# Optimization experiments

Hardware: AMD Instinct MI355X
Metric: run time of the kernel (lower is better)

Reference implementation:

```python
import jax, jax.numpy as jnp
import numpy as np
from jax import lax

N, C_IN, L = 32, 8, 4096
C_LAT, K_EMB, E_DIM = 64, 512, 64
KSZ, STRIDE, PAD = 4, 2, 2


def setup_inputs() -> dict:
    key = jax.random.key(0)
    ks = jax.random.split(key, 6)
    s_conv = 1.0 / np.sqrt(C_IN * KSZ)
    s_tconv = 1.0 / np.sqrt(C_LAT * KSZ)
    return {
        "x": jax.random.normal(ks[0], (N, C_IN, L), jnp.float32),
        "conv_w": jax.random.normal(ks[1], (C_LAT, C_IN, KSZ), jnp.float32) * s_conv,
        "conv_b": jax.random.normal(ks[2], (C_LAT,), jnp.float32) * s_conv,
        "codebook": jax.random.normal(ks[3], (K_EMB, E_DIM), jnp.float32),
        "tconv_w": jax.random.normal(ks[4], (C_LAT, C_IN, KSZ), jnp.float32) * s_tconv,
        "tconv_b": jax.random.normal(ks[5], (C_IN,), jnp.float32) * s_tconv,
    }


def _encode(x, conv_w, conv_b):
    z = lax.conv_general_dilated(
        x, conv_w, window_strides=(STRIDE,), padding=[(PAD, PAD)],
        dimension_numbers=("NCH", "OIH", "NCH"))
    return z + conv_b[None, :, None]


def _quantize(z_e, codebook):
    n, c, l = z_e.shape
    z_flat = z_e.transpose(0, 2, 1).reshape(-1, c)          # (n*l, c)
    z_sq = jnp.sum(z_flat * z_flat, axis=1, keepdims=True)  # (n*l, 1)
    cb_sq = jnp.sum(codebook * codebook, axis=1)            # (k,)
    dist = z_sq + cb_sq[None, :] - 2.0 * (z_flat @ codebook.T)
    indices = jnp.argmin(dist, axis=-1)                     # (n*l,)
    z_q = codebook[indices].reshape(n, l, c).transpose(0, 2, 1)
    return z_q, indices.reshape(n, l)


def _decode(z_q, tconv_w, tconv_b):
    # torch ConvTranspose1d == conv with lhs-dilated input, flipped/transposed kernel
    w_t = jnp.flip(tconv_w, -1).transpose(1, 0, 2)          # (out, in, k)
    x_rec = lax.conv_general_dilated(
        z_q, w_t, window_strides=(1,),
        padding=[(KSZ - 1 - PAD, KSZ - 1 - PAD)],
        lhs_dilation=(STRIDE,),
        dimension_numbers=("NCH", "OIH", "NCH"))
    return x_rec + tconv_b[None, :, None]


def reference(x, conv_w, conv_b, codebook, tconv_w, tconv_b):
    z_e = _encode(x, conv_w, conv_b)            # (N, C_LAT, L/2+1)
    z_q, indices = _quantize(z_e, codebook)
    x_recon = _decode(z_q, tconv_w, tconv_b)    # (N, C_IN, L)
    return x_recon, z_e, z_q, indices
```

## Files before the change

### kernel.cpp

```cpp
#include <hip/hip_runtime.h>
#include <stdint.h>

#define N_B   32
#define C_INN 8
#define L_IN  4096
#define C_LAT 64
#define K_EMB 512
#define E_DIM 64
#define L_OUT 2049
#define M_ROWS (N_B * L_OUT)

#define SZ_XREC (N_B * C_INN * L_IN)
#define SZ_ZE   (N_B * C_LAT * L_OUT)
#define OFF_XREC 0
#define OFF_ZE   (SZ_XREC)
#define OFF_ZQ   (OFF_ZE + SZ_ZE)
#define OFF_IDX  (OFF_ZQ + SZ_ZE)

typedef short short8 __attribute__((ext_vector_type(8)));
typedef float f32x4  __attribute__((ext_vector_type(4)));

__device__ __forceinline__ unsigned short rne16(float f) {
    unsigned u = __float_as_uint(f);
    return (unsigned short)((u + 0x7FFFu + ((u >> 16) & 1u)) >> 16);
}
__device__ __forceinline__ float frombits16(unsigned short h) {
    return __uint_as_float(((unsigned)h) << 16);
}
__device__ __forceinline__ unsigned orderbits(float f) {
    unsigned u = __float_as_uint(f);
    return u ^ ((unsigned)((int)u >> 31) | 0x80000000u);
}

__global__ __launch_bounds__(256) void prep_kernel(
    const float* __restrict__ cb, unsigned short* __restrict__ frag,
    float* __restrict__ cbh)
{
    const int ntile = blockIdx.x;
    const int t     = threadIdx.x;
    const int lane  = t & 63;
    const int ks    = (t >> 6) & 1;
    const int h     = t >> 7;
    const int code  = ntile * 16 + (lane & 15);
    const int k0    = ks * 32 + (lane >> 4) * 8;

    const float* src = cb + (size_t)code * E_DIM + k0;
    unsigned short out[8];
#pragma unroll
    for (int j = 0; j < 8; ++j) {
        const float v = src[j];
        const unsigned short hb = rne16(v);
        out[j] = h ? rne16(v - frombits16(hb)) : hb;
    }
    short8 v8;
#pragma unroll
    for (int j = 0; j < 8; ++j) v8[j] = (short)out[j];
    short8* dst = (short8*)(frag + (((size_t)(ntile * 2 + ks) * 2 + h) * 512 + lane * 8));
    *dst = v8;

    if (t < 16) {
        const int c2 = ntile * 16 + t;
        const float4* cp = (const float4*)(cb + (size_t)c2 * E_DIM);
        float s = 0.0f;
#pragma unroll
        for (int d = 0; d < E_DIM / 4; ++d) {
            float4 v = cp[d];
            s += v.x * v.x + v.y * v.y + v.z * v.z + v.w * v.w;
        }
        cbh[c2] = 0.5f * s;
    }
}

__global__ __launch_bounds__(256, 3) void quantize_kernel(
    const float* __restrict__ x, const float* __restrict__ conv_w,
    const float* __restrict__ conv_b, const float* __restrict__ cb,
    const unsigned short* __restrict__ frag, const float* __restrict__ cbh_ws,
    float* __restrict__ z_e, float* __restrict__ z_q,
    float* __restrict__ idx_out)
{
    __shared__ float s_z[E_DIM][66];
    __shared__ float s_cbh[K_EMB];
    __shared__ unsigned s_cand[64][68];
    __shared__ float s_znorm[64];
    __shared__ unsigned s_mstar[64];
    __shared__ unsigned long long s_final[64];
    __shared__ unsigned s_list[256];
    __shared__ int s_cnt;

    const int tid  = threadIdx.x;
    const int wave = tid >> 6;
    const int lane = tid & 63;
    const int p    = wave >> 1;
    const int h    = wave & 1;

    s_cbh[tid]       = cbh_ws[tid];
    s_cbh[tid + 256] = cbh_ws[tid + 256];
    if (tid < 64) s_final[tid] = ~0ULL;
    if (tid == 0) s_cnt = 0;

    const int  row    = lane;
    const int  r      = blockIdx.x * 64 + row;
    const bool active = (r < M_ROWS);
    const unsigned rr = active ? (unsigned)r : 0u;
    const unsigned n  = rr / 2049u;
    const unsigned tt = rr - n * 2049u;

    {
        const float* xrow = x + (size_t)n * (C_INN * L_IN);
        float xv[C_INN][4];
        const bool fast = (tt >= 1 && tt <= 2047);
        if (fast) {
#pragma unroll
            for (int ci = 0; ci < C_INN; ++ci) {
                float4 v = *(const float4*)(xrow + ci * L_IN + (2 * (int)tt - 2));
                xv[ci][0] = v.x; xv[ci][1] = v.y; xv[ci][2] = v.z; xv[ci][3] = v.w;
            }
        } else {
#pragma unroll
            for (int ci = 0; ci < C_INN; ++ci) {
#pragma unroll
                for (int k = 0; k < 4; ++k) {
                    int xi = 2 * (int)tt - 2 + k;
                    int xc = min(max(xi, 0), L_IN - 1);
                    float v = xrow[ci * L_IN + xc];
                    xv[ci][k] = (xi >= 0 && xi < L_IN) ? v : 0.0f;
                }
            }
        }
        float* zcol = z_e + (size_t)n * (C_LAT * L_OUT) + tt;
#pragma unroll
        for (int j = 0; j < 16; ++j) {
            const int c = wave * 16 + j;
            float a = conv_b[c];
#pragma unroll
            for (int ci = 0; ci < C_INN; ++ci) {
                const float* wp = conv_w + (c * C_INN + ci) * 4;
#pragma unroll
                for (int k = 0; k < 4; ++k) a += xv[ci][k] * wp[k];
            }
            s_z[c][row] = a;
            if (active) zcol[(size_t)c * L_OUT] = a;
        }
    }
    __syncthreads();

    if (tid < 64) {
        float s = 0.0f;
#pragma unroll 8
        for (int c = 0; c < E_DIM; ++c) {
            const float v = s_z[c][tid];
            s += v * v;
        }
        s_znorm[tid] = 0.5f * s + 1.0f;
    }

    const int m = lane & 15, q = lane >> 4;
    short8 Ah[2][2], Al[2][2];
#pragma unroll
    for (int st = 0; st < 2; ++st) {
        const int arow = p * 32 + st * 16 + m;
#pragma unroll
        for (int ks = 0; ks < 2; ++ks) {
#pragma unroll
            for (int j = 0; j < 8; ++j) {
                const float v = -s_z[ks * 32 + q * 8 + j][arow];
                const unsigned short hb = rne16(v);
                Ah[st][ks][j] = (short)hb;
                Al[st][ks][j] = (short)rne16(v - frombits16(hb));
            }
        }
    }
    __syncthreads();

    float Kn[2][4];
#pragma unroll
    for (int st = 0; st < 2; ++st)
#pragma unroll
        for (int r4 = 0; r4 < 4; ++r4)
            Kn[st][r4] = s_znorm[p * 32 + st * 16 + q * 4 + r4];

    unsigned ca[2][4], cb2[2][4];
#pragma unroll
    for (int st = 0; st < 2; ++st)
#pragma unroll
        for (int r4 = 0; r4 < 4; ++r4) { ca[st][r4] = 0xFFFFFFFFu; cb2[st][r4] = 0xFFFFFFFFu; }

    const short8* B8 = (const short8*)frag;
    short8 Bc[4], Bn[4];
    {
        const int base = (h * 16) * 256 + lane;
#pragma unroll
        for (int v = 0; v < 4; ++v) Bc[v] = B8[base + v * 64];
    }

    for (int t = 0; t < 16; ++t) {
        if (t < 15) {
            const int base = (h * 16 + t + 1) * 256 + lane;
#pragma unroll
            for (int v = 0; v < 4; ++v) Bn[v] = B8[base + v * 64];
        }
        const int code = (h * 16 + t) * 16 + m;
        const float chv = s_cbh[code];

        f32x4 accA = {chv + Kn[0][0], chv + Kn[0][1], chv + Kn[0][2], chv + Kn[0][3]};
        f32x4 accB = {chv + Kn[1][0], chv + Kn[1][1], chv + Kn[1][2], chv + Kn[1][3]};
        accA = __builtin_amdgcn_mfma_f32_16x16x32_bf16(Ah[0][0], Bc[0], accA, 0, 0, 0);
        accB = __builtin_amdgcn_mfma_f32_16x16x32_bf16(Ah[1][0], Bc[0], accB, 0, 0, 0);
        accA = __builtin_amdgcn_mfma_f32_16x16x32_bf16(Ah[0][0], Bc[1], accA, 0, 0, 0);
        accB = __builtin_amdgcn_mfma_f32_16x16x32_bf16(Ah[1][0], Bc[1], accB, 0, 0, 0);
        accA = __builtin_amdgcn_mfma_f32_16x16x32_bf16(Al[0][0], Bc[0], accA, 0, 0, 0);
        accB = __builtin_amdgcn_mfma_f32_16x16x32_bf16(Al[1][0], Bc[0], accB, 0, 0, 0);
        accA = __builtin_amdgcn_mfma_f32_16x16x32_bf16(Ah[0][1], Bc[2], accA, 0, 0, 0);
        accB = __builtin_amdgcn_mfma_f32_16x16x32_bf16(Ah[1][1], Bc[2], accB, 0, 0, 0);
        accA = __builtin_amdgcn_mfma_f32_16x16x32_bf16(Ah[0][1], Bc[3], accA, 0, 0, 0);
        accB = __builtin_amdgcn_mfma_f32_16x16x32_bf16(Ah[1][1], Bc[3], accB, 0, 0, 0);
        accA = __builtin_amdgcn_mfma_f32_16x16x32_bf16(Al[0][1], Bc[2], accA, 0, 0, 0);
        accB = __builtin_amdgcn_mfma_f32_16x16x32_bf16(Al[1][1], Bc[2], accB, 0, 0, 0);

#pragma unroll
        for (int st = 0; st < 2; ++st) {
            const f32x4 acc = st ? accB : accA;
#pragma unroll
            for (int r4 = 0; r4 < 4; ++r4) {
                const unsigned xx = (__float_as_uint(acc[r4]) & 0xFFFFFFF0u) | (unsigned)t;
                const unsigned mx = max(ca[st][r4], xx);
                ca[st][r4]  = min(ca[st][r4], xx);
                cb2[st][r4] = min(cb2[st][r4], mx);
            }
        }
#pragma unroll
        for (int v = 0; v < 4; ++v) Bc[v] = Bn[v];
    }

#pragma unroll
    for (int st = 0; st < 2; ++st)
#pragma unroll
        for (int r4 = 0; r4 < 4; ++r4) {
            const int rw = p * 32 + st * 16 + q * 4 + r4;
            s_cand[rw][h * 32 + 2 * m + 0] = ca[st][r4];
            s_cand[rw][h * 32 + 2 * m + 1] = cb2[st][r4];
        }
    __syncthreads();

    if (tid < 64) {
        unsigned mn = 0xFFFFFFFFu;
#pragma unroll 8
        for (int i = 0; i < 64; ++i) mn = min(mn, s_cand[tid][i]);
        s_mstar[tid] = mn & 0xFFFFFFF0u;
    }
    __syncthreads();

    {
        const int rw  = tid >> 2;
        const float thr = __uint_as_float(s_mstar[rw]) + 0.02f;
#pragma unroll
        for (int j = 0; j < 16; ++j) {
            const int sl = (tid & 3) * 16 + j;
            const unsigned cand = s_cand[rw][sl];
            const float fd = __uint_as_float(cand & 0xFFFFFFF0u);
            if (fd <= thr) {
                const unsigned code =
                    (((unsigned)(sl >> 5) * 16u + (cand & 15u)) * 16u) +
                    (unsigned)((sl >> 1) & 15);
                const int pos = atomicAdd(&s_cnt, 1);
                if (pos < 256) {
                    s_list[pos] = ((unsigned)rw << 9) | code;
                } else {
                    const float4* c4 = (const float4*)(cb + (size_t)code * E_DIM);
                    float dot = 0.0f;
#pragma unroll
                    for (int d4 = 0; d4 < 16; ++d4) {
                        const float4 cv = c4[d4];
                        dot += s_z[d4 * 4 + 0][rw] * cv.x +
                               s_z[d4 * 4 + 1][rw] * cv.y +
                               s_z[d4 * 4 + 2][rw] * cv.z +
                               s_z[d4 * 4 + 3][rw] * cv.w;
                    }
                    const float mex = s_cbh[code] - dot;
                    const unsigned long long px =
                        ((unsigned long long)orderbits(mex) << 32) | code;
                    atomicMin(&s_final[rw], px);
                }
            }
        }
    }
    __syncthreads();

    {
        const int nk = min(s_cnt, 256);
        for (int e = tid; e < nk; e += 256) {
            const unsigned ent = s_list[e];
            const int rw = (int)(ent >> 9);
            const unsigned code = ent & 511u;
            const float4* c4 = (const float4*)(cb + (size_t)code * E_DIM);
            float dot = 0.0f;
#pragma unroll
            for (int d4 = 0; d4 < 16; ++d4) {
                const float4 cv = c4[d4];
                dot += s_z[d4 * 4 + 0][rw] * cv.x +
                       s_z[d4 * 4 + 1][rw] * cv.y +
                       s_z[d4 * 4 + 2][rw] * cv.z +
                       s_z[d4 * 4 + 3][rw] * cv.w;
            }
            const float mex = s_cbh[code] - dot;
            const unsigned long long px =
                ((unsigned long long)orderbits(mex) << 32) | code;
            atomicMin(&s_final[rw], px);
        }
    }
    __syncthreads();

    if (active) {
        const unsigned fk = (unsigned)s_final[row];
        const float4* csel = (const float4*)(cb + (size_t)fk * E_DIM);
        float* zq = z_q + (size_t)n * (C_LAT * L_OUT) + tt;
#pragma unroll
        for (int j4 = 0; j4 < 4; ++j4) {
            const float4 cv = csel[wave * 4 + j4];
            const int c = wave * 16 + j4 * 4;
            zq[(size_t)(c + 0) * L_OUT] = cv.x;
            zq[(size_t)(c + 1) * L_OUT] = cv.y;
            zq[(size_t)(c + 2) * L_OUT] = cv.z;
            zq[(size_t)(c + 3) * L_OUT] = cv.w;
        }
        if (tid < 64) idx_out[r] = (float)fk;
    }
}

__global__ __launch_bounds__(128) void decode_kernel(
    const float* __restrict__ zq, const float* __restrict__ w,
    const float* __restrict__ b, float* __restrict__ xr)
{
    const int blk   = blockIdx.x;
    const int chunk = blk & 15;
    const int cog   = (blk >> 4) & 1;
    const int n     = blk >> 5;
    const int s     = chunk * 128 + threadIdx.x;
    const int co0   = cog * 4;

    const float* zn = zq + (size_t)n * (C_LAT * L_OUT) + s;
    float e[4], o[4];
#pragma unroll
    for (int j = 0; j < 4; ++j) { e[j] = b[co0 + j]; o[j] = e[j]; }

#pragma unroll 4
    for (int ci = 0; ci < C_LAT; ++ci) {
        const float z0 = zn[(size_t)ci * L_OUT];
        const float z1 = zn[(size_t)ci * L_OUT + 1];
        const float* wp = w + (ci * C_INN + co0) * 4;
#pragma unroll
        for (int j = 0; j < 4; ++j) {
            e[j] += z0 * wp[4 * j + 2] + z1 * wp[4 * j + 0];
            o[j] += z0 * wp[4 * j + 3] + z1 * wp[4 * j + 1];
        }
    }

#pragma unroll
    for (int j = 0; j < 4; ++j) {
        float* xrow = xr + ((size_t)(n * C_INN + co0 + j)) * L_IN;
        *(float2*)(xrow + 2 * s) = make_float2(e[j], o[j]);
    }
}

extern "C" void kernel_launch(void* const* d_in, const int* in_sizes, int n_in,
                              void* d_out, int out_size, void* d_ws, size_t ws_size,
                              hipStream_t stream) {
    const float* x        = (const float*)d_in[0];
    const float* conv_w   = (const float*)d_in[1];
    const float* conv_b   = (const float*)d_in[2];
    const float* codebook = (const float*)d_in[3];
    const float* tconv_w  = (const float*)d_in[4];
    const float* tconv_b  = (const float*)d_in[5];

    float* out   = (float*)d_out;
    float* x_rec = out + OFF_XREC;
    float* z_e   = out + OFF_ZE;
    float* z_q   = out + OFF_ZQ;
    float* idxs  = out + OFF_IDX;

    unsigned short* frag = (unsigned short*)d_ws;
    float*          cbh  = (float*)(frag + 65536);

    prep_kernel<<<32, 256, 0, stream>>>(codebook, frag, cbh);
    quantize_kernel<<<(M_ROWS + 63) / 64, 256, 0, stream>>>(
        x, conv_w, conv_b, codebook, frag, cbh, z_e, z_q, idxs);
    decode_kernel<<<1024, 128, 0, stream>>>(z_q, tconv_w, tconv_b, x_rec);
}
```

Baseline: 131.1 us.

## Double waves per block, split codebook four ways, drop shared z tile

The quantize kernel moves from 256 to 512 threads (8 waves). Each wave computes 8 latent channels and covers a quarter of the codebook rather than a half. The shared s_z tile is removed: the row norm is built from per-wave partial sums, and the A fragments and exact-rescoring dot products re-read z_e from global memory, which is expected to hit L2. The goal is less LDS per block and more parallel waves, at the cost of strided global reloads and a wider candidate merge (128 slots per row).

```diff
diff --git a/kernel.cpp b/kernel.cpp
--- a/kernel.cpp
+++ b/kernel.cpp
@@ -71,17 +71,19 @@
     }
 }
 
-__global__ __launch_bounds__(256, 3) void quantize_kernel(
+#define WAVES 8
+__global__ __launch_bounds__(512, 8) void quantize_kernel(
     const float* __restrict__ x, const float* __restrict__ conv_w,
     const float* __restrict__ conv_b, const float* __restrict__ cb,
     const unsigned short* __restrict__ frag, const float* __restrict__ cbh_ws,
     float* __restrict__ z_e, float* __restrict__ z_q,
     float* __restrict__ idx_out)
 {
-    __shared__ float s_z[E_DIM][66];
     __shared__ float s_cbh[K_EMB];
-    __shared__ unsigned s_cand[64][68];
+    __shared__ unsigned s_cand[64][133];
+    __shared__ float s_pn[64][WAVES];
     __shared__ float s_znorm[64];
+    __shared__ unsigned s_rowoff[64];
     __shared__ unsigned s_mstar[64];
     __shared__ unsigned long long s_final[64];
     __shared__ unsigned s_list[256];
@@ -90,20 +92,21 @@
     const int tid  = threadIdx.x;
     const int wave = tid >> 6;
     const int lane = tid & 63;
-    const int p    = wave >> 1;
-    const int h    = wave & 1;
-
-    s_cbh[tid]       = cbh_ws[tid];
-    s_cbh[tid + 256] = cbh_ws[tid + 256];
+    const int wb   = __builtin_amdgcn_readfirstlane(wave);
+    const int p    = wb >> 2;
+    const int hq   = wb & 3;
+
+    s_cbh[tid] = cbh_ws[tid];
     if (tid < 64) s_final[tid] = ~0ULL;
     if (tid == 0) s_cnt = 0;
 
     const int  row    = lane;
     const int  r      = blockIdx.x * 64 + row;
     const bool active = (r < M_ROWS);
-    const unsigned rr = active ? (unsigned)r : 0u;
+    const unsigned rr = active ? (unsigned)r : (unsigned)(blockIdx.x * 64);
     const unsigned n  = rr / 2049u;
     const unsigned tt = rr - n * 2049u;
+    const unsigned zoff = n * (C_LAT * L_OUT) + tt;
 
     {
         const float* xrow = x + (size_t)n * (C_INN * L_IN);
@@ -127,10 +130,11 @@
                 }
             }
         }
-        float* zcol = z_e + (size_t)n * (C_LAT * L_OUT) + tt;
-#pragma unroll
-        for (int j = 0; j < 16; ++j) {
-            const int c = wave * 16 + j;
+        float* zcol = z_e + zoff;
+        float pn = 0.0f;
+#pragma unroll
+        for (int j = 0; j < 8; ++j) {
+            const int c = wb * 8 + j;
             float a = conv_b[c];
 #pragma unroll
             for (int ci = 0; ci < C_INN; ++ci) {
@@ -138,32 +142,33 @@
 #pragma unroll
                 for (int k = 0; k < 4; ++k) a += xv[ci][k] * wp[k];
             }
-            s_z[c][row] = a;
+            pn += a * a;
             if (active) zcol[(size_t)c * L_OUT] = a;
         }
+        s_pn[row][wb] = pn;
+        if (wb == 0) s_rowoff[row] = zoff;
     }
     __syncthreads();
 
     if (tid < 64) {
         float s = 0.0f;
-#pragma unroll 8
-        for (int c = 0; c < E_DIM; ++c) {
-            const float v = s_z[c][tid];
-            s += v * v;
-        }
+#pragma unroll
+        for (int w2 = 0; w2 < WAVES; ++w2) s += s_pn[tid][w2];
         s_znorm[tid] = 0.5f * s + 1.0f;
     }
 
     const int m = lane & 15, q = lane >> 4;
+    const unsigned ro0 = s_rowoff[p * 32 + m];
+    const unsigned ro1 = s_rowoff[p * 32 + 16 + m];
     short8 Ah[2][2], Al[2][2];
 #pragma unroll
     for (int st = 0; st < 2; ++st) {
-        const int arow = p * 32 + st * 16 + m;
+        const float* zb = z_e + (st ? ro1 : ro0);
 #pragma unroll
         for (int ks = 0; ks < 2; ++ks) {
 #pragma unroll
             for (int j = 0; j < 8; ++j) {
-                const float v = -s_z[ks * 32 + q * 8 + j][arow];
+                const float v = -zb[(size_t)((ks * 32 + q * 8 + j) * L_OUT)];
                 const unsigned short hb = rne16(v);
                 Ah[st][ks][j] = (short)hb;
                 Al[st][ks][j] = (short)rne16(v - frombits16(hb));
@@ -188,18 +193,18 @@
     const short8* B8 = (const short8*)frag;
     short8 Bc[4], Bn[4];
     {
-        const int base = (h * 16) * 256 + lane;
+        const int base = (hq * 8) * 256 + lane;
 #pragma unroll
         for (int v = 0; v < 4; ++v) Bc[v] = B8[base + v * 64];
     }
 
-    for (int t = 0; t < 16; ++t) {
-        if (t < 15) {
-            const int base = (h * 16 + t + 1) * 256 + lane;
+    for (int t = 0; t < 8; ++t) {
+        if (t < 7) {
+            const int base = (hq * 8 + t + 1) * 256 + lane;
 #pragma unroll
             for (int v = 0; v < 4; ++v) Bn[v] = B8[base + v * 64];
         }
-        const int code = (h * 16 + t) * 16 + m;
+        const int code = (hq * 8 + t) * 16 + m;
         const float chv = s_cbh[code];
 
         f32x4 accA = {chv + Kn[0][0], chv + Kn[0][1], chv + Kn[0][2], chv + Kn[0][3]};
@@ -237,30 +242,31 @@
 #pragma unroll
         for (int r4 = 0; r4 < 4; ++r4) {
             const int rw = p * 32 + st * 16 + q * 4 + r4;
-            s_cand[rw][h * 32 + 2 * m + 0] = ca[st][r4];
-            s_cand[rw][h * 32 + 2 * m + 1] = cb2[st][r4];
+            s_cand[rw][hq * 32 + 2 * m + 0] = ca[st][r4];
+            s_cand[rw][hq * 32 + 2 * m + 1] = cb2[st][r4];
         }
     __syncthreads();
 
     if (tid < 64) {
         unsigned mn = 0xFFFFFFFFu;
 #pragma unroll 8
-        for (int i = 0; i < 64; ++i) mn = min(mn, s_cand[tid][i]);
+        for (int i = 0; i < 128; ++i) mn = min(mn, s_cand[tid][i]);
         s_mstar[tid] = mn & 0xFFFFFFF0u;
     }
     __syncthreads();
 
     {
-        const int rw  = tid >> 2;
+        const int rw  = tid >> 3;
         const float thr = __uint_as_float(s_mstar[rw]) + 0.02f;
+        const float* zp = z_e + s_rowoff[rw];
 #pragma unroll
         for (int j = 0; j < 16; ++j) {
-            const int sl = (tid & 3) * 16 + j;
+            const int sl = (tid & 7) * 16 + j;
             const unsigned cand = s_cand[rw][sl];
             const float fd = __uint_as_float(cand & 0xFFFFFFF0u);
             if (fd <= thr) {
                 const unsigned code =
-                    (((unsigned)(sl >> 5) * 16u + (cand & 15u)) * 16u) +
+                    (((unsigned)(sl >> 5) * 8u + (cand & 15u)) * 16u) +
                     (unsigned)((sl >> 1) & 15);
                 const int pos = atomicAdd(&s_cnt, 1);
                 if (pos < 256) {
@@ -271,10 +277,10 @@
 #pragma unroll
                     for (int d4 = 0; d4 < 16; ++d4) {
                         const float4 cv = c4[d4];
-                        dot += s_z[d4 * 4 + 0][rw] * cv.x +
-                               s_z[d4 * 4 + 1][rw] * cv.y +
-                               s_z[d4 * 4 + 2][rw] * cv.z +
-                               s_z[d4 * 4 + 3][rw] * cv.w;
+                        dot += zp[(size_t)((4 * d4 + 0) * L_OUT)] * cv.x +
+                               zp[(size_t)((4 * d4 + 1) * L_OUT)] * cv.y +
+                               zp[(size_t)((4 * d4 + 2) * L_OUT)] * cv.z +
+                               zp[(size_t)((4 * d4 + 3) * L_OUT)] * cv.w;
                     }
                     const float mex = s_cbh[code] - dot;
                     const unsigned long long px =
@@ -288,19 +294,20 @@
 
     {
         const int nk = min(s_cnt, 256);
-        for (int e = tid; e < nk; e += 256) {
+        for (int e = tid; e < nk; e += 512) {
             const unsigned ent = s_list[e];
             const int rw = (int)(ent >> 9);
             const unsigned code = ent & 511u;
+            const float* zp = z_e + s_rowoff[rw];
             const float4* c4 = (const float4*)(cb + (size_t)code * E_DIM);
             float dot = 0.0f;
 #pragma unroll
             for (int d4 = 0; d4 < 16; ++d4) {
                 const float4 cv = c4[d4];
-                dot += s_z[d4 * 4 + 0][rw] * cv.x +
-                       s_z[d4 * 4 + 1][rw] * cv.y +
-                       s_z[d4 * 4 + 2][rw] * cv.z +
-                       s_z[d4 * 4 + 3][rw] * cv.w;
+                dot += zp[(size_t)((4 * d4 + 0) * L_OUT)] * cv.x +
+                       zp[(size_t)((4 * d4 + 1) * L_OUT)] * cv.y +
+                       zp[(size_t)((4 * d4 + 2) * L_OUT)] * cv.z +
+                       zp[(size_t)((4 * d4 + 3) * L_OUT)] * cv.w;
             }
             const float mex = s_cbh[code] - dot;
             const unsigned long long px =
@@ -313,11 +320,11 @@
     if (active) {
         const unsigned fk = (unsigned)s_final[row];
         const float4* csel = (const float4*)(cb + (size_t)fk * E_DIM);
-        float* zq = z_q + (size_t)n * (C_LAT * L_OUT) + tt;
-#pragma unroll
-        for (int j4 = 0; j4 < 4; ++j4) {
-            const float4 cv = csel[wave * 4 + j4];
-            const int c = wave * 16 + j4 * 4;
+        float* zq = z_q + zoff;
+#pragma unroll
+        for (int j4 = 0; j4 < 2; ++j4) {
+            const float4 cv = csel[wb * 2 + j4];
+            const int c = wb * 8 + j4 * 4;
             zq[(size_t)(c + 0) * L_OUT] = cv.x;
             zq[(size_t)(c + 1) * L_OUT] = cv.y;
             zq[(size_t)(c + 2) * L_OUT] = cv.z;
@@ -382,7 +389,7 @@
     float*          cbh  = (float*)(frag + 65536);
 
     prep_kernel<<<32, 256, 0, stream>>>(codebook, frag, cbh);
-    quantize_kernel<<<(M_ROWS + 63) / 64, 256, 0, stream>>>(
+    quantize_kernel<<<(M_ROWS + 63) / 64, 512, 0, stream>>>(
         x, conv_w, conv_b, codebook, frag, cbh, z_e, z_q, idxs);
     decode_kernel<<<1024, 128, 0, stream>>>(z_q, tconv_w, tconv_b, x_rec);
 }
```

Measured after the change: 301.9 us. 130% more time.

## Shrink quantize tile to 32 rows per block and raise occupancy

Applied to the files above, without the earlier changes.

Halves the rows per quantize block from 64 to 32, so each wave handles one 16-row MFMA subtile instead of two. Launch bounds rise to 7 waves per SIMD, and shared memory shrinks so more blocks can be resident. The z-norm now comes from per-group partial sums gathered during the conv, and the MFMA chain is split into two independent accumulators to shorten dependencies. The risks are reloading the codebook fragments from global memory twice as often per row and register pressure under the tighter launch bound. Bounds checks are dropped because M_ROWS divides evenly by 32.

```diff
diff --git a/kernel.cpp b/kernel.cpp
--- a/kernel.cpp
+++ b/kernel.cpp
@@ -71,39 +71,41 @@
     }
 }
 
-__global__ __launch_bounds__(256, 3) void quantize_kernel(
+__global__ __launch_bounds__(256, 7) void quantize_kernel(
     const float* __restrict__ x, const float* __restrict__ conv_w,
     const float* __restrict__ conv_b, const float* __restrict__ cb,
     const unsigned short* __restrict__ frag, const float* __restrict__ cbh_ws,
     float* __restrict__ z_e, float* __restrict__ z_q,
     float* __restrict__ idx_out)
 {
-    __shared__ float s_z[E_DIM][66];
+    __shared__ float s_z[E_DIM][33];
+    __shared__ unsigned s_cand[32][67];
     __shared__ float s_cbh[K_EMB];
-    __shared__ unsigned s_cand[64][68];
-    __shared__ float s_znorm[64];
-    __shared__ unsigned s_mstar[64];
-    __shared__ unsigned long long s_final[64];
+    __shared__ float s_pn[32][8];
+    __shared__ float s_znorm[32];
+    __shared__ unsigned s_mstar[32];
+    __shared__ unsigned long long s_final[32];
     __shared__ unsigned s_list[256];
     __shared__ int s_cnt;
 
     const int tid  = threadIdx.x;
     const int wave = tid >> 6;
     const int lane = tid & 63;
-    const int p    = wave >> 1;
-    const int h    = wave & 1;
+    const int wb   = __builtin_amdgcn_readfirstlane(wave);
+    const int sp   = wb >> 1;
+    const int h    = wb & 1;
 
     s_cbh[tid]       = cbh_ws[tid];
     s_cbh[tid + 256] = cbh_ws[tid + 256];
-    if (tid < 64) s_final[tid] = ~0ULL;
+    if (tid < 32) s_final[tid] = ~0ULL;
     if (tid == 0) s_cnt = 0;
 
-    const int  row    = lane;
-    const int  r      = blockIdx.x * 64 + row;
-    const bool active = (r < M_ROWS);
-    const unsigned rr = active ? (unsigned)r : 0u;
-    const unsigned n  = rr / 2049u;
-    const unsigned tt = rr - n * 2049u;
+    const int row = tid & 31;
+    const int g   = tid >> 5;
+    const int r   = blockIdx.x * 32 + row;
+    const unsigned n  = (unsigned)r / 2049u;
+    const unsigned tt = (unsigned)r - n * 2049u;
+    const unsigned zoff = n * (C_LAT * L_OUT) + tt;
 
     {
         const float* xrow = x + (size_t)n * (C_INN * L_IN);
@@ -127,10 +129,11 @@
                 }
             }
         }
-        float* zcol = z_e + (size_t)n * (C_LAT * L_OUT) + tt;
-#pragma unroll
-        for (int j = 0; j < 16; ++j) {
-            const int c = wave * 16 + j;
+        float* zcol = z_e + zoff;
+        float pn = 0.0f;
+#pragma unroll
+        for (int j = 0; j < 8; ++j) {
+            const int c = g * 8 + j;
             float a = conv_b[c];
 #pragma unroll
             for (int ci = 0; ci < C_INN; ++ci) {
@@ -138,52 +141,44 @@
 #pragma unroll
                 for (int k = 0; k < 4; ++k) a += xv[ci][k] * wp[k];
             }
+            pn += a * a;
             s_z[c][row] = a;
-            if (active) zcol[(size_t)c * L_OUT] = a;
-        }
-    }
-    __syncthreads();
-
-    if (tid < 64) {
+            zcol[(size_t)c * L_OUT] = a;
+        }
+        s_pn[row][g] = pn;
+    }
+    __syncthreads();
+
+    if (tid < 32) {
         float s = 0.0f;
-#pragma unroll 8
-        for (int c = 0; c < E_DIM; ++c) {
-            const float v = s_z[c][tid];
-            s += v * v;
-        }
+#pragma unroll
+        for (int g2 = 0; g2 < 8; ++g2) s += s_pn[tid][g2];
         s_znorm[tid] = 0.5f * s + 1.0f;
     }
 
     const int m = lane & 15, q = lane >> 4;
-    short8 Ah[2][2], Al[2][2];
-#pragma unroll
-    for (int st = 0; st < 2; ++st) {
-        const int arow = p * 32 + st * 16 + m;
-#pragma unroll
-        for (int ks = 0; ks < 2; ++ks) {
-#pragma unroll
-            for (int j = 0; j < 8; ++j) {
-                const float v = -s_z[ks * 32 + q * 8 + j][arow];
-                const unsigned short hb = rne16(v);
-                Ah[st][ks][j] = (short)hb;
-                Al[st][ks][j] = (short)rne16(v - frombits16(hb));
-            }
-        }
-    }
-    __syncthreads();
-
-    float Kn[2][4];
-#pragma unroll
-    for (int st = 0; st < 2; ++st)
-#pragma unroll
-        for (int r4 = 0; r4 < 4; ++r4)
-            Kn[st][r4] = s_znorm[p * 32 + st * 16 + q * 4 + r4];
-
-    unsigned ca[2][4], cb2[2][4];
-#pragma unroll
-    for (int st = 0; st < 2; ++st)
-#pragma unroll
-        for (int r4 = 0; r4 < 4; ++r4) { ca[st][r4] = 0xFFFFFFFFu; cb2[st][r4] = 0xFFFFFFFFu; }
+    const int arow = sp * 16 + m;
+    short8 Ah[2], Al[2];
+#pragma unroll
+    for (int ks = 0; ks < 2; ++ks) {
+#pragma unroll
+        for (int j = 0; j < 8; ++j) {
+            const float v = -s_z[ks * 32 + q * 8 + j][arow];
+            const unsigned short hb = rne16(v);
+            Ah[ks][j] = (short)hb;
+            Al[ks][j] = (short)rne16(v - frombits16(hb));
+        }
+    }
+    __syncthreads();
+
+    float Kn[4];
+#pragma unroll
+    for (int r4 = 0; r4 < 4; ++r4)
+        Kn[r4] = s_znorm[sp * 16 + q * 4 + r4];
+
+    unsigned ca[4], cb2[4];
+#pragma unroll
+    for (int r4 = 0; r4 < 4; ++r4) { ca[r4] = 0xFFFFFFFFu; cb2[r4] = 0xFFFFFFFFu; }
 
     const short8* B8 = (const short8*)frag;
     short8 Bc[4], Bn[4];
@@ -202,47 +197,36 @@
         const int code = (h * 16 + t) * 16 + m;
         const float chv = s_cbh[code];
 
-        f32x4 accA = {chv + Kn[0][0], chv + Kn[0][1], chv + Kn[0][2], chv + Kn[0][3]};
-        f32x4 accB = {chv + Kn[1][0], chv + Kn[1][1], chv + Kn[1][2], chv + Kn[1][3]};
-        accA = __builtin_amdgcn_mfma_f32_16x16x32_bf16(Ah[0][0], Bc[0], accA, 0, 0, 0);
-        accB = __builtin_amdgcn_mfma_f32_16x16x32_bf16(Ah[1][0], Bc[0], accB, 0, 0, 0);
-        accA = __builtin_amdgcn_mfma_f32_16x16x32_bf16(Ah[0][0], Bc[1], accA, 0, 0, 0);
-        accB = __builtin_amdgcn_mfma_f32_16x16x32_bf16(Ah[1][0], Bc[1], accB, 0, 0, 0);
-        accA = __builtin_amdgcn_mfma_f32_16x16x32_bf16(Al[0][0], Bc[0], accA, 0, 0, 0);
-        accB = __builtin_amdgcn_mfma_f32_16x16x32_bf16(Al[1][0], Bc[0], accB, 0, 0, 0);
-        accA = __builtin_amdgcn_mfma_f32_16x16x32_bf16(Ah[0][1], Bc[2], accA, 0, 0, 0);
-        accB = __builtin_amdgcn_mfma_f32_16x16x32_bf16(Ah[1][1], Bc[2], accB, 0, 0, 0);
-        accA = __builtin_amdgcn_mfma_f32_16x16x32_bf16(Ah[0][1], Bc[3], accA, 0, 0, 0);
-        accB = __builtin_amdgcn_mfma_f32_16x16x32_bf16(Ah[1][1], Bc[3], accB, 0, 0, 0);
-        accA = __builtin_amdgcn_mfma_f32_16x16x32_bf16(Al[0][1], Bc[2], accA, 0, 0, 0);
-        accB = __builtin_amdgcn_mfma_f32_16x16x32_bf16(Al[1][1], Bc[2], accB, 0, 0, 0);
-
-#pragma unroll
-        for (int st = 0; st < 2; ++st) {
-            const f32x4 acc = st ? accB : accA;
-#pragma unroll
-            for (int r4 = 0; r4 < 4; ++r4) {
-                const unsigned xx = (__float_as_uint(acc[r4]) & 0xFFFFFFF0u) | (unsigned)t;
-                const unsigned mx = max(ca[st][r4], xx);
-                ca[st][r4]  = min(ca[st][r4], xx);
-                cb2[st][r4] = min(cb2[st][r4], mx);
-            }
+        f32x4 acc1 = {chv + Kn[0], chv + Kn[1], chv + Kn[2], chv + Kn[3]};
+        f32x4 acc2 = {0.0f, 0.0f, 0.0f, 0.0f};
+        acc1 = __builtin_amdgcn_mfma_f32_16x16x32_bf16(Ah[0], Bc[0], acc1, 0, 0, 0);
+        acc2 = __builtin_amdgcn_mfma_f32_16x16x32_bf16(Ah[1], Bc[2], acc2, 0, 0, 0);
+        acc1 = __builtin_amdgcn_mfma_f32_16x16x32_bf16(Ah[0], Bc[1], acc1, 0, 0, 0);
+        acc2 = __builtin_amdgcn_mfma_f32_16x16x32_bf16(Ah[1], Bc[3], acc2, 0, 0, 0);
+        acc1 = __builtin_amdgcn_mfma_f32_16x16x32_bf16(Al[0], Bc[0], acc1, 0, 0, 0);
+        acc2 = __builtin_amdgcn_mfma_f32_16x16x32_bf16(Al[1], Bc[2], acc2, 0, 0, 0);
+
+#pragma unroll
+        for (int r4 = 0; r4 < 4; ++r4) {
+            const float d = acc1[r4] + acc2[r4];
+            const unsigned xx = (__float_as_uint(d) & 0xFFFFFFF0u) | (unsigned)t;
+            const unsigned mx = max(ca[r4], xx);
+            ca[r4]  = min(ca[r4], xx);
+            cb2[r4] = min(cb2[r4], mx);
         }
 #pragma unroll
         for (int v = 0; v < 4; ++v) Bc[v] = Bn[v];
     }
 
 #pragma unroll
-    for (int st = 0; st < 2; ++st)
-#pragma unroll
-        for (int r4 = 0; r4 < 4; ++r4) {
-            const int rw = p * 32 + st * 16 + q * 4 + r4;
-            s_cand[rw][h * 32 + 2 * m + 0] = ca[st][r4];
-            s_cand[rw][h * 32 + 2 * m + 1] = cb2[st][r4];
-        }
-    __syncthreads();
-
-    if (tid < 64) {
+    for (int r4 = 0; r4 < 4; ++r4) {
+        const int rw = sp * 16 + q * 4 + r4;
+        s_cand[rw][h * 32 + 2 * m + 0] = ca[r4];
+        s_cand[rw][h * 32 + 2 * m + 1] = cb2[r4];
+    }
+    __syncthreads();
+
+    if (tid < 32) {
         unsigned mn = 0xFFFFFFFFu;
 #pragma unroll 8
         for (int i = 0; i < 64; ++i) mn = min(mn, s_cand[tid][i]);
@@ -251,11 +235,11 @@
     __syncthreads();
 
     {
-        const int rw  = tid >> 2;
+        const int rw  = tid >> 3;
         const float thr = __uint_as_float(s_mstar[rw]) + 0.02f;
 #pragma unroll
-        for (int j = 0; j < 16; ++j) {
-            const int sl = (tid & 3) * 16 + j;
+        for (int j = 0; j < 8; ++j) {
+            const int sl = (tid & 7) * 8 + j;
             const unsigned cand = s_cand[rw][sl];
             const float fd = __uint_as_float(cand & 0xFFFFFFF0u);
             if (fd <= thr) {
@@ -310,20 +294,20 @@
     }
     __syncthreads();
 
-    if (active) {
+    {
         const unsigned fk = (unsigned)s_final[row];
         const float4* csel = (const float4*)(cb + (size_t)fk * E_DIM);
-        float* zq = z_q + (size_t)n * (C_LAT * L_OUT) + tt;
-#pragma unroll
-        for (int j4 = 0; j4 < 4; ++j4) {
-            const float4 cv = csel[wave * 4 + j4];
-            const int c = wave * 16 + j4 * 4;
+        float* zq = z_q + zoff;
+#pragma unroll
+        for (int j4 = 0; j4 < 2; ++j4) {
+            const float4 cv = csel[g * 2 + j4];
+            const int c = g * 8 + j4 * 4;
             zq[(size_t)(c + 0) * L_OUT] = cv.x;
             zq[(size_t)(c + 1) * L_OUT] = cv.y;
             zq[(size_t)(c + 2) * L_OUT] = cv.z;
             zq[(size_t)(c + 3) * L_OUT] = cv.w;
         }
-        if (tid < 64) idx_out[r] = (float)fk;
+        if (tid < 32) idx_out[r] = (float)fk;
     }
 }
 
@@ -382,7 +366,7 @@
     float*          cbh  = (float*)(frag + 65536);
 
     prep_kernel<<<32, 256, 0, stream>>>(codebook, frag, cbh);
-    quantize_kernel<<<(M_ROWS + 63) / 64, 256, 0, stream>>>(
+    quantize_kernel<<<M_ROWS / 32, 256, 0, stream>>>(
         x, conv_w, conv_b, codebook, frag, cbh, z_e, z_q, idxs);
     decode_kernel<<<1024, 128, 0, stream>>>(z_q, tconv_w, tconv_b, x_rec);
 }
```

After: 237.3 us. 81.0% more time.
